# Performance work log

Measured on AMD Instinct MI355X. Metric: run time of the kernel, lower is better.

The kernel has to match this reference:

```python
import jax, jax.numpy as jnp
import numpy as np

B, C_IN, C_MID, C_OUT, L = 32, 8, 128, 128, 512
T, DT = 50, 0.5
K = T // 2 + 1  # 26
DN = ('NCH', 'OIH', 'NCH')

def conv1d_same(x, w, b):
    # zero-padded 'SAME' Conv1d, kernel size 3
    y = jax.lax.conv_general_dilated(x, w, (1,), 'SAME', dimension_numbers=DN)
    return y + b[None, :, None]

def setup_inputs() -> dict:
    key = jax.random.key(0)
    ks = jax.random.split(key, 32)
    def n(k, shape, s=0.1):
        return jax.random.normal(k, shape, dtype=jnp.float32) * s
    inp = {}
    inp['x'] = jax.random.normal(ks[0], (B, C_IN, L), dtype=jnp.float32)
    # omega encoder (3 convs + ReLU)
    inp['ow1'] = n(ks[1], (C_MID, C_IN, 3));  inp['ob1'] = jnp.zeros((C_MID,), jnp.float32)
    inp['ow2'] = n(ks[2], (C_MID, C_MID, 3)); inp['ob2'] = jnp.zeros((C_MID,), jnp.float32)
    inp['ow3'] = n(ks[3], (C_OUT, C_MID, 3)); inp['ob3'] = jnp.zeros((C_OUT,), jnp.float32)
    # alpha encoder
    inp['aw1'] = n(ks[4], (C_MID, C_IN, 3));  inp['ab1'] = jnp.zeros((C_MID,), jnp.float32)
    inp['aw2'] = n(ks[5], (C_MID, C_MID, 3)); inp['ab2'] = jnp.zeros((C_MID,), jnp.float32)
    inp['aw3'] = n(ks[6], (C_OUT, C_MID, 3)); inp['ab3'] = jnp.zeros((C_OUT,), jnp.float32)
    # hy encoder (4 convs, last Tanh)
    inp['hw1'] = n(ks[7], (C_MID, C_IN, 3));  inp['hb1'] = jnp.zeros((C_MID,), jnp.float32)
    inp['hw2'] = n(ks[8], (C_MID, C_MID, 3)); inp['hb2'] = jnp.zeros((C_MID,), jnp.float32)
    inp['hw3'] = n(ks[9], (C_MID, C_MID, 3)); inp['hb3'] = jnp.zeros((C_MID,), jnp.float32)
    inp['hw4'] = n(ks[10], (C_OUT, C_MID, 3)); inp['hb4'] = jnp.zeros((C_OUT,), jnp.float32)
    # cell circular conv weight (no bias)
    inp['wy'] = n(ks[11], (C_OUT, C_OUT, 3))
    # linear readout
    inp['fct'] = n(ks[12], (K, T))                     # fc_time: T -> K, no bias
    inp['rw1'] = n(ks[13], (64, K * C_OUT)); inp['rb1'] = jnp.zeros((64,), jnp.float32)
    inp['rw2'] = n(ks[14], (32, 64));        inp['rb2'] = jnp.zeros((32,), jnp.float32)
    inp['rw3'] = n(ks[15], (1, 32));         inp['rb3'] = jnp.zeros((1,), jnp.float32)
    return inp

def reference(x, ow1, ob1, ow2, ob2, ow3, ob3,
              aw1, ab1, aw2, ab2, aw3, ab3,
              hw1, hb1, hw2, hb2, hw3, hb3, hw4, hb4,
              wy, fct, rw1, rb1, rw2, rb2, rw3, rb3):
    relu = jax.nn.relu
    omega = relu(conv1d_same(relu(conv1d_same(relu(conv1d_same(x, ow1, ob1)), ow2, ob2)), ow3, ob3))
    alpha = relu(conv1d_same(relu(conv1d_same(relu(conv1d_same(x, aw1, ab1)), aw2, ab2)), aw3, ab3))
    h = relu(conv1d_same(x, hw1, hb1))
    h = relu(conv1d_same(h, hw2, hb2))
    h = relu(conv1d_same(h, hw3, hb3))
    hy0 = jnp.tanh(conv1d_same(h, hw4, hb4))          # (B, C_OUT, L)
    hz0 = jnp.zeros_like(hy0)

    def circ_conv(h):
        # circular padding of 1 on each side, then VALID conv (matches padding_mode='circular')
        hp = jnp.concatenate([h[..., -1:], h, h[..., :1]], axis=-1)
        return jax.lax.conv_general_dilated(hp, wy, (1,), 'VALID', dimension_numbers=DN)

    def step(carry, _):
        hy, hz = carry
        spring = jnp.tanh(circ_conv(hy))
        hz = hz + DT * (spring - omega * hy - alpha * hz)
        hy = hy + DT * hz
        return (hy, hz), hy

    (_, _), ys = jax.lax.scan(step, (hy0, hz0), None, length=T)
    y_seq = jnp.transpose(ys, (1, 0, 2, 3))           # (B, T, C_OUT, L)

    # linear readout: fc_time over T, mean over L, MLP
    fft = jnp.einsum('btcl,kt->bkcl', y_seq, fct)     # (B, K, C_OUT, L)
    feat = fft.reshape(B, K * C_OUT, L).mean(axis=2)  # (B, K*C_OUT)
    h1 = relu(feat @ rw1.T + rb1)
    h2 = relu(h1 @ rw2.T + rb2)
    logits = h2 @ rw3.T + rb3                         # (B, 1)
    return logits, y_seq
```

## Files before the change

kernel.cpp:

```cpp
#include <hip/hip_runtime.h>
#include <math.h>

#define YB (50*128*512)
#define YT (128*512)
#define DTc 0.5f

typedef __attribute__((ext_vector_type(8))) short bf16x8;
typedef __attribute__((ext_vector_type(4))) float f32x4;

__device__ __forceinline__ unsigned short f2bf(float f) {
    unsigned int u = __builtin_bit_cast(unsigned int, f);
    u += 0x7fffu + ((u >> 16) & 1u);
    return (unsigned short)(u >> 16);
}
__device__ __forceinline__ float bf2f(unsigned short h) {
    unsigned int u = ((unsigned int)h) << 16;
    return __builtin_bit_cast(float, u);
}

__device__ __forceinline__ float tanh_fast(float x) {
    float ax = fabsf(x);
    float e  = __expf(-2.f * ax);
    float r  = (1.f - e) * __builtin_amdgcn_rcpf(1.f + e);
    return __builtin_copysignf(r, x);
}

__device__ __forceinline__ void lds_sync() {
    asm volatile("s_waitcnt lgkmcnt(0)" ::: "memory");
    __builtin_amdgcn_sched_barrier(0);
    __builtin_amdgcn_s_barrier();
    __builtin_amdgcn_sched_barrier(0);
}

__device__ __forceinline__ uint4 dpp_k1(uint4 a0, uint4 a2) {
    uint4 r;
    int t;
    t = __builtin_amdgcn_update_dpp(0, (int)a0.x, 0x101, 0xF, 0xF, false);
    r.x = (unsigned)__builtin_amdgcn_update_dpp(t, (int)a2.x, 0x111, 0xF, 0xF, false);
    t = __builtin_amdgcn_update_dpp(0, (int)a0.y, 0x101, 0xF, 0xF, false);
    r.y = (unsigned)__builtin_amdgcn_update_dpp(t, (int)a2.y, 0x111, 0xF, 0xF, false);
    t = __builtin_amdgcn_update_dpp(0, (int)a0.z, 0x101, 0xF, 0xF, false);
    r.z = (unsigned)__builtin_amdgcn_update_dpp(t, (int)a2.z, 0x111, 0xF, 0xF, false);
    t = __builtin_amdgcn_update_dpp(0, (int)a0.w, 0x101, 0xF, 0xF, false);
    r.w = (unsigned)__builtin_amdgcn_update_dpp(t, (int)a2.w, 0x111, 0xF, 0xF, false);
    return r;
}

struct WSrc { const float* p[11]; };
__global__ void wprep_all_k(WSrc s, float* __restrict__ wt) {
    int idx = blockIdx.x * 256 + threadIdx.x;
    if (idx < 9216) {
        int wsel = idx / 3072, r = idx % 3072;
        int row = r >> 7, co = r & 127;
        int ci = row / 3, k = row - ci * 3;
        wt[idx] = s.p[wsel][(co * 8 + ci) * 3 + k];
    } else if (idx < 9216 + 589824) {
        int q = idx - 9216;
        int cv = q / 49152, r = q % 49152;
        int co = r / 384, kap = r % 384;
        int k = kap >> 7;
        int ci = ((kap >> 5) & 3) * 32 + (kap & 31);
        const int selmap[12] = {10, 7, 8, 9, 3, 3, 4, 4, 5, 5, 6, 6};
        float w = s.p[selmap[cv]][(co * 128 + ci) * 3 + k];
        unsigned short hv = f2bf(w);
        unsigned short ov = ((cv >= 4) && (cv & 1)) ? f2bf(w - bf2f(hv)) : hv;
        ((unsigned short*)(wt + 9216))[q] = ov;
    }
}

struct Job { const float* src; float* dst; const float* wt; const float* bias; int sbs, dbs, act; };
struct Jobs3 { Job j[3]; };

__global__ __launch_bounds__(256) void conv8x3_k(Jobs3 js) {
    int jb = blockIdx.y % 3;
    Job jo = js.j[jb];
    int b = blockIdx.z, tile = blockIdx.x, tid = threadIdx.x;
    int l0 = tile * 64;
    int tl4 = (tid & 15) * 4;
    int co0 = (tid >> 4) * 8;
    __shared__ float xs[8 * 68];
    __shared__ float wsh[24 * 128];
    const float* sb = jo.src + (size_t)b * jo.sbs;
    for (int idx = tid; idx < 8 * 66; idx += 256) {
        int ci = idx / 66, ll = idx - ci * 66;
        int gl = l0 - 1 + ll;
        xs[ci * 68 + ll] = (gl >= 0 && gl < 512) ? sb[ci * 512 + gl] : 0.f;
    }
    for (int idx = tid; idx < 24 * 128; idx += 256) wsh[idx] = jo.wt[idx];
    __syncthreads();
    float acc[8][4] = {};
    #pragma unroll
    for (int ci = 0; ci < 8; ++ci) {
        float x6[6];
        #pragma unroll
        for (int j = 0; j < 6; ++j) x6[j] = xs[ci * 68 + tl4 + j];
        #pragma unroll
        for (int k = 0; k < 3; ++k) {
            float w8[8];
            #pragma unroll
            for (int i = 0; i < 8; ++i) w8[i] = wsh[(ci * 3 + k) * 128 + co0 + i];
            #pragma unroll
            for (int i = 0; i < 8; ++i)
                #pragma unroll
                for (int j = 0; j < 4; ++j)
                    acc[i][j] = fmaf(w8[i], x6[k + j], acc[i][j]);
        }
    }
    #pragma unroll
    for (int i = 0; i < 8; ++i) {
        int co = co0 + i;
        float bv = jo.bias[co];
        float4 o;
        o.x = fmaxf(acc[i][0] + bv, 0.f);
        o.y = fmaxf(acc[i][1] + bv, 0.f);
        o.z = fmaxf(acc[i][2] + bv, 0.f);
        o.w = fmaxf(acc[i][3] + bv, 0.f);
        *(float4*)(jo.dst + (size_t)b * jo.dbs + (size_t)co * 512 + l0 + tl4) = o;
    }
}

struct UJob { const float* src; float* dst; const unsigned short* whi;
              const unsigned short* wlo; const float* bias; int sbs, dbs; };
struct UJobs3 { UJob j[3]; };

__global__ __launch_bounds__(512) void uconv_k(UJobs3 js) {
    UJob jo = js.j[blockIdx.z];
    int tile = blockIdx.x, b = blockIdx.y;
    int tid = threadIdx.x, lane = tid & 63, wid = tid >> 6;
    int lr = lane & 15, kg = lane >> 4;
    int co = wid * 16 + lr;
    int l0 = tile * 32;
    bool dual = (jo.wlo != nullptr);

    __shared__ float stage[128 * 40];
    __shared__ uint4 hiX[34 * 16];
    __shared__ uint4 loX[34 * 16];

    const bf16x8* wph = (const bf16x8*)(jo.whi + (size_t)co * 384);
    bf16x8 Bh[12];
    #pragma unroll
    for (int s = 0; s < 12; ++s) Bh[s] = wph[s * 4 + kg];

    const float* sb = jo.src + (size_t)b * jo.sbs;
    for (int i = tid; i < 1280; i += 512) {
        int c = i / 10, p4 = (i - c * 10) * 4;
        int l = l0 - 4 + p4;
        f32x4 v;
        if (l >= 0 && l <= 508) {
            v = *(const f32x4*)(sb + (size_t)c * 512 + l);
        } else {
            #pragma unroll
            for (int e = 0; e < 4; ++e) {
                int le = l + e;
                v[e] = (le >= 0 && le < 512) ? sb[(size_t)c * 512 + le] : 0.f;
            }
        }
        *(f32x4*)(stage + c * 40 + p4) = v;
    }
    __syncthreads();
    for (int i = tid; i < 34 * 16; i += 512) {
        int h = i >> 4, c8 = i & 15;
        unsigned short ph[8], pl[8];
        #pragma unroll
        for (int q = 0; q < 8; ++q) {
            float x = stage[(c8 * 8 + q) * 40 + h + 3];
            unsigned short hv = f2bf(x);
            ph[q] = hv;
            pl[q] = f2bf(x - bf2f(hv));
        }
        int sx = h * 16 + (c8 ^ (h & 7));
        hiX[sx] = *(uint4*)ph;
        if (dual) loX[sx] = *(uint4*)pl;
    }
    __syncthreads();

    f32x4 acc[2];
    acc[0] = (f32x4){0.f, 0.f, 0.f, 0.f};
    acc[1] = (f32x4){0.f, 0.f, 0.f, 0.f};
    __builtin_amdgcn_s_setprio(1);
    if (dual) {
        const bf16x8* wpl = (const bf16x8*)(jo.wlo + (size_t)co * 384);
        bf16x8 blc = wpl[kg];
        #pragma unroll
        for (int s = 0; s < 12; ++s) {
            bf16x8 Bl = blc;
            if (s < 11) blc = wpl[(s + 1) * 4 + kg];
            int k = s >> 2;
            int chunk = (s & 3) * 4 + kg;
            #pragma unroll
            for (int lt = 0; lt < 2; ++lt) {
                int arow = 16 * lt + lr + k;
                int ai = arow * 16 + ((arow & 7) ^ chunk);
                bf16x8 ah = __builtin_bit_cast(bf16x8, hiX[ai]);
                bf16x8 al = __builtin_bit_cast(bf16x8, loX[ai]);
                acc[lt] = __builtin_amdgcn_mfma_f32_16x16x32_bf16(ah, Bh[s], acc[lt], 0, 0, 0);
                acc[lt] = __builtin_amdgcn_mfma_f32_16x16x32_bf16(al, Bh[s], acc[lt], 0, 0, 0);
                acc[lt] = __builtin_amdgcn_mfma_f32_16x16x32_bf16(ah, Bl,    acc[lt], 0, 0, 0);
            }
        }
    } else {
        #pragma unroll
        for (int s = 0; s < 12; ++s) {
            int k = s >> 2;
            int chunk = (s & 3) * 4 + kg;
            #pragma unroll
            for (int lt = 0; lt < 2; ++lt) {
                int arow = 16 * lt + lr + k;
                bf16x8 ah = __builtin_bit_cast(bf16x8, hiX[arow * 16 + ((arow & 7) ^ chunk)]);
                acc[lt] = __builtin_amdgcn_mfma_f32_16x16x32_bf16(ah, Bh[s], acc[lt], 0, 0, 0);
            }
        }
    }
    __builtin_amdgcn_s_setprio(0);

    float bv = jo.bias[co];
    #pragma unroll
    for (int lt = 0; lt < 2; ++lt) {
        float v[4];
        #pragma unroll
        for (int j = 0; j < 4; ++j) v[j] = fmaxf(acc[lt][j] + bv, 0.f);
        *(f32x4*)(jo.dst + (size_t)b * jo.dbs + (size_t)co * 512 + l0 + 16 * lt + 4 * kg) = *(f32x4*)v;
    }
}

__global__ __launch_bounds__(512) void mconv_k(
    const float* __restrict__ src, int sbs,
    float* __restrict__ dst, int dbs,
    const unsigned short* __restrict__ w2,
    const float* __restrict__ bias,
    unsigned short* __restrict__ hyt)
{
    int tile = blockIdx.x, b = blockIdx.y;
    int tid = threadIdx.x, lane = tid & 63, wid = tid >> 6;
    int lr = lane & 15, kg = lane >> 4;
    int co = wid * 16 + lr;
    int l0 = tile * 32;

    __shared__ float stage[128 * 40];
    __shared__ uint4 hyX[34 * 16];

    bf16x8 Bw[12];
    {
        const bf16x8* wp = (const bf16x8*)(w2 + (size_t)co * 384);
        #pragma unroll
        for (int s = 0; s < 12; ++s) Bw[s] = wp[s * 4 + kg];
    }

    const float* sb = src + (size_t)b * sbs;
    for (int i = tid; i < 1280; i += 512) {
        int c = i / 10, p4 = (i - c * 10) * 4;
        int l = l0 - 4 + p4;
        f32x4 v;
        if (l >= 0 && l <= 508) {
            v = *(const f32x4*)(sb + (size_t)c * 512 + l);
        } else {
            #pragma unroll
            for (int e = 0; e < 4; ++e) {
                int le = l + e;
                v[e] = (le >= 0 && le < 512) ? sb[(size_t)c * 512 + le] : 0.f;
            }
        }
        *(f32x4*)(stage + c * 40 + p4) = v;
    }
    __syncthreads();
    for (int i = tid; i < 34 * 16; i += 512) {
        int h = i >> 4, c8 = i & 15;
        unsigned short pk[8];
        #pragma unroll
        for (int q = 0; q < 8; ++q) pk[q] = f2bf(stage[(c8 * 8 + q) * 40 + h + 3]);
        hyX[h * 16 + (c8 ^ (h & 7))] = *(uint4*)pk;
    }
    __syncthreads();

    f32x4 acc[2];
    acc[0] = (f32x4){0.f, 0.f, 0.f, 0.f};
    acc[1] = (f32x4){0.f, 0.f, 0.f, 0.f};
    __builtin_amdgcn_s_setprio(1);
    #pragma unroll
    for (int s = 0; s < 12; ++s) {
        int k = s >> 2;
        int chunk = (s & 3) * 4 + kg;
        bf16x8 Bf = Bw[s];
        #pragma unroll
        for (int lt = 0; lt < 2; ++lt) {
            int arow = 16 * lt + lr + k;
            bf16x8 a = __builtin_bit_cast(bf16x8, hyX[arow * 16 + ((arow & 7) ^ chunk)]);
            acc[lt] = __builtin_amdgcn_mfma_f32_16x16x32_bf16(a, Bf, acc[lt], 0, 0, 0);
        }
    }
    __builtin_amdgcn_s_setprio(0);

    float bv = bias[co];
    float vv[2][4];
    #pragma unroll
    for (int lt = 0; lt < 2; ++lt) {
        #pragma unroll
        for (int j = 0; j < 4; ++j)
            vv[lt][j] = tanh_fast(acc[lt][j] + bv);
        *(f32x4*)(dst + (size_t)b * dbs + (size_t)co * 512 + l0 + 16 * lt + 4 * kg) = *(f32x4*)vv[lt];
    }

    lds_sync();
    {
        unsigned short* t16 = (unsigned short*)hyX;
        #pragma unroll
        for (int lt = 0; lt < 2; ++lt)
            #pragma unroll
            for (int j = 0; j < 4; ++j)
                t16[(16 * lt + 4 * kg + j) * 128 + co] = f2bf(vv[lt][j]);
        lds_sync();
        int row = tid >> 4, c8 = tid & 15;
        ((uint4*)hyt)[((size_t)b * 512 + l0 + row) * 16 + c8] =
            ((uint4*)hyX)[row * 16 + c8];
    }
}

__global__ __launch_bounds__(512, 2) void chunk_k(
    const unsigned short* __restrict__ hyt_in,
    unsigned short* __restrict__ hyt_out,
    const float* __restrict__ hy_in,
    const float* __restrict__ hz_in,
    float* __restrict__ hz_out,
    const float* __restrict__ omega, const float* __restrict__ alpha,
    const unsigned short* __restrict__ w2,
    float* __restrict__ ybase,
    float* __restrict__ part, int t0, int ns)
{
    int tile = blockIdx.x, b = blockIdx.y;
    int tid = threadIdx.x, lane = tid & 63, wid = tid >> 6;
    int lr = lane & 15, kg = lane >> 4;
    int co = wid * 16 + lr;
    int l0 = tile * 32;

    __shared__ uint4 hySd[2][800];
    __shared__ float ytmp[2 * 4608];

    bf16x8 Bw[12];
    {
        const bf16x8* wp = (const bf16x8*)(w2 + (size_t)co * 384);
        #pragma unroll
        for (int s = 0; s < 12; ++s) Bw[s] = wp[s * 4 + kg];
    }

    f32x4 hyR[3], hzR[3], omR[3], alR[3];

    {
        const uint4* hsrc = (const uint4*)hyt_in + (size_t)b * 8192;
        for (int i = tid; i < 800; i += 512) {
            int h = i >> 4, c8 = i & 15;
            int l = (l0 - 9 + h) & 511;
            hySd[0][h * 16 + (c8 ^ (h & 7))] = hsrc[l * 16 + c8];
        }
    }
    {
        const float* src = hy_in + (size_t)b * YB;
        size_t ob = (size_t)b * 65536 + (size_t)co * 512;
        #pragma unroll
        for (int lt = 0; lt < 3; ++lt) {
            int l = (l0 - 8 + 16 * lt + 4 * kg) & 511;
            hyR[lt] = *(const f32x4*)(src + (size_t)co * 512 + l);
            omR[lt] = *(const f32x4*)(omega + ob + l);
            alR[lt] = *(const f32x4*)(alpha + ob + l);
            if (t0 > 0) hzR[lt] = *(const f32x4*)(hz_in + ob + l);
            else        hzR[lt] = (f32x4){0.f, 0.f, 0.f, 0.f};
        }
    }
    __syncthreads();

    for (int i = 0; i < ns; ++i) {
        const uint4* hc = &hySd[i & 1][0];
        unsigned short* hn16 = (unsigned short*)&hySd[(i + 1) & 1][0];
        float* yt = ytmp + (i & 1) * 4608;

        f32x4 acc[3];
        #pragma unroll
        for (int lt = 0; lt < 3; ++lt) acc[lt] = (f32x4){0.f, 0.f, 0.f, 0.f};
        __builtin_amdgcn_s_setprio(1);
        #pragma unroll
        for (int cs = 0; cs < 4; ++cs) {
            int chunk = cs * 4 + kg;
            bf16x8 B0 = Bw[cs], B1 = Bw[cs + 4], B2 = Bw[cs + 8];
            #pragma unroll
            for (int lt = 0; lt < 3; ++lt) {
                int r0 = 16 * lt + lr;
                int r2 = r0 + 2;
                uint4 a0 = hc[r0 * 16 + ((r0 & 7) ^ chunk)];
                uint4 a2 = hc[r2 * 16 + ((r2 & 7) ^ chunk)];
                acc[lt] = __builtin_amdgcn_mfma_f32_16x16x32_bf16(
                    __builtin_bit_cast(bf16x8, a0), B0, acc[lt], 0, 0, 0);
                acc[lt] = __builtin_amdgcn_mfma_f32_16x16x32_bf16(
                    __builtin_bit_cast(bf16x8, a2), B2, acc[lt], 0, 0, 0);
                uint4 a1 = dpp_k1(a0, a2);
                acc[lt] = __builtin_amdgcn_mfma_f32_16x16x32_bf16(
                    __builtin_bit_cast(bf16x8, a1), B1, acc[lt], 0, 0, 0);
            }
        }
        __builtin_amdgcn_s_setprio(0);

        float lsum = 0.f;
        #pragma unroll
        for (int lt = 0; lt < 3; ++lt) {
            #pragma unroll
            for (int j = 0; j < 4; ++j) {
                float spring = tanh_fast(acc[lt][j]);
                float zn = hzR[lt][j] + DTc * (spring - omR[lt][j] * hyR[lt][j] - alR[lt][j] * hzR[lt][j]);
                float hn = hyR[lt][j] + DTc * zn;
                hzR[lt][j] = zn;
                hyR[lt][j] = hn;
            }
            bool valid = (lt == 0) ? (kg >= 2) : (lt == 2) ? (kg < 2) : true;
            int r0 = 16 * lt + 4 * kg;
            if (valid) {
                *(f32x4*)(yt + co * 36 + (r0 - 8)) = hyR[lt];
                lsum += hyR[lt][0] + hyR[lt][1] + hyR[lt][2] + hyR[lt][3];
                if (i == ns - 1)
                    *(f32x4*)(hz_out + (size_t)b * 65536 + (size_t)co * 512 + l0 + (r0 - 8)) = hzR[lt];
            }
            #pragma unroll
            for (int j = 0; j < 4; ++j) {
                int rr = r0 + j + 1;
                int sidx = rr * 128 + (((co >> 3) ^ (rr & 7)) << 3) + (co & 7);
                hn16[sidx] = f2bf(hyR[lt][j]);
            }
        }
        lsum += __shfl_xor(lsum, 16);
        lsum += __shfl_xor(lsum, 32);
        if (kg == 0) part[(((size_t)b * 50 + t0 + i) * 128 + co) * 16 + tile] = lsum;

        lds_sync();

        {
            float* yrow = ybase + (size_t)b * YB + (size_t)i * YT;
            int cs2 = wid * 16 + (lane >> 3);
            int lq = (lane & 7) * 4;
            #pragma unroll
            for (int cq = 0; cq < 2; ++cq) {
                int c2 = cs2 + cq * 8;
                f32x4 v = *(const f32x4*)(yt + c2 * 36 + lq);
                *(f32x4*)(yrow + (size_t)c2 * 512 + l0 + lq) = v;
            }
        }
    }

    {
        const uint4* hl = &hySd[ns & 1][0];
        int row = tid >> 4, c8 = tid & 15;
        int h = row + 9;
        ((uint4*)hyt_out)[((size_t)b * 512 + l0 + row) * 16 + c8] =
            hl[h * 16 + (c8 ^ (h & 7))];
    }
}

__global__ __launch_bounds__(256) void readout_k(
    const float* __restrict__ part, const float* __restrict__ fct,
    const float* __restrict__ rw1, const float* __restrict__ rb1,
    const float* __restrict__ rw2, const float* __restrict__ rb2,
    const float* __restrict__ rw3, const float* __restrict__ rb3,
    float* __restrict__ out)
{
    int b = blockIdx.x, tid = threadIdx.x;
    __shared__ float ybar[50 * 128];
    __shared__ float feat[26 * 128];
    __shared__ float h1[64];
    __shared__ float h2[32];
    for (int idx = tid; idx < 50 * 128; idx += 256) {
        const float* p = part + ((size_t)b * 6400 + idx) * 16;
        float s = 0.f;
        #pragma unroll
        for (int q = 0; q < 16; ++q) s += p[q];
        ybar[idx] = s * (1.f / 512.f);
    }
    __syncthreads();
    for (int idx = tid; idx < 26 * 128; idx += 256) {
        int k = idx >> 7, c = idx & 127;
        float s = 0.f;
        for (int t = 0; t < 50; ++t) s += fct[k * 50 + t] * ybar[t * 128 + c];
        feat[idx] = s;
    }
    __syncthreads();
    {
        int j = tid >> 2, q = tid & 3;
        float s = 0.f;
        const float* r = rw1 + (size_t)j * 3328 + q * 832;
        const float* f = feat + q * 832;
        for (int i = 0; i < 832; ++i) s += f[i] * r[i];
        s += __shfl_xor(s, 1);
        s += __shfl_xor(s, 2);
        if (q == 0) h1[j] = fmaxf(s + rb1[j], 0.f);
    }
    __syncthreads();
    if (tid < 32) {
        float s = 0.f;
        for (int i = 0; i < 64; ++i) s += h1[i] * rw2[tid * 64 + i];
        h2[tid] = fmaxf(s + rb2[tid], 0.f);
    }
    __syncthreads();
    if (tid == 0) {
        float s = 0.f;
        for (int i = 0; i < 32; ++i) s += h2[i] * rw3[i];
        out[b] = s + rb3[0];
    }
}

extern "C" void kernel_launch(void* const* d_in, const int* in_sizes, int n_in,
                              void* d_out, int out_size, void* d_ws, size_t ws_size,
                              hipStream_t stream)
{
    const float* x   = (const float*)d_in[0];
    const float* ow1 = (const float*)d_in[1];  const float* ob1 = (const float*)d_in[2];
    const float* ow2 = (const float*)d_in[3];  const float* ob2 = (const float*)d_in[4];
    const float* ow3 = (const float*)d_in[5];  const float* ob3 = (const float*)d_in[6];
    const float* aw1 = (const float*)d_in[7];  const float* ab1 = (const float*)d_in[8];
    const float* aw2 = (const float*)d_in[9];  const float* ab2 = (const float*)d_in[10];
    const float* aw3 = (const float*)d_in[11]; const float* ab3 = (const float*)d_in[12];
    const float* hw1 = (const float*)d_in[13]; const float* hb1 = (const float*)d_in[14];
    const float* hw2 = (const float*)d_in[15]; const float* hb2 = (const float*)d_in[16];
    const float* hw3 = (const float*)d_in[17]; const float* hb3 = (const float*)d_in[18];
    const float* hw4 = (const float*)d_in[19]; const float* hb4 = (const float*)d_in[20];
    const float* wy  = (const float*)d_in[21];
    const float* fct = (const float*)d_in[22];
    const float* rw1 = (const float*)d_in[23]; const float* rb1 = (const float*)d_in[24];
    const float* rw2 = (const float*)d_in[25]; const float* rb2 = (const float*)d_in[26];
    const float* rw3 = (const float*)d_in[27]; const float* rb3 = (const float*)d_in[28];

    float* out  = (float*)d_out;
    float* yout = out + 32;
    float* ws   = (float*)d_ws;

    float* OMEGA = ws;
    float* ALPHA = ws + 2097152;
    float* WT    = ws + 4194304;
    float* PART  = ws + 4498432;
    float* HZ0   = ws + 7775232;
    float* HZ1   = ws + 9872384;
    unsigned short* HYT0 = (unsigned short*)(ws + 11969536);
    unsigned short* HYT1 = (unsigned short*)(ws + 13018112);

    float* To1 = yout + 44 * YT;
    float* Ta1 = yout + 45 * YT;
    float* Th1 = yout + 46 * YT;
    float* To2 = yout + 47 * YT;
    float* Ta2 = yout + 43 * YT;
    float* Th2 = yout + 49 * YT;
    float* Th3 = yout + 42 * YT;
    float* HY0 = yout + 48 * YT;

    float* OW1T = WT + 0;  float* AW1T = WT + 3072;  float* HW1T = WT + 6144;
    unsigned short* U16 = (unsigned short*)(WT + 9216);
    unsigned short* W2WY = U16;
    unsigned short* W2H2 = U16 + 49152;
    unsigned short* W2H3 = U16 + 98304;
    unsigned short* W2H4 = U16 + 147456;
    unsigned short* OW2H = U16 + 196608;  unsigned short* OW2L = U16 + 245760;
    unsigned short* OW3H = U16 + 294912;  unsigned short* OW3L = U16 + 344064;
    unsigned short* AW2H = U16 + 393216;  unsigned short* AW2L = U16 + 442368;
    unsigned short* AW3H = U16 + 491520;  unsigned short* AW3L = U16 + 540672;

    WSrc wsrc;
    wsrc.p[0] = ow1; wsrc.p[1] = aw1; wsrc.p[2] = hw1;
    wsrc.p[3] = ow2; wsrc.p[4] = ow3; wsrc.p[5] = aw2; wsrc.p[6] = aw3;
    wsrc.p[7] = hw2; wsrc.p[8] = hw3; wsrc.p[9] = hw4; wsrc.p[10] = wy;
    wprep_all_k<<<2340, 256, 0, stream>>>(wsrc, WT);

    Jobs3 d1 = {{ {x, To1, OW1T, ob1, 4096, YB, 1},
                  {x, Ta1, AW1T, ab1, 4096, YB, 1},
                  {x, Th1, HW1T, hb1, 4096, YB, 1} }};
    conv8x3_k<<<dim3(8, 3, 32), 256, 0, stream>>>(d1);

    UJobs3 u2 = {{ {To1, To2, OW2H, OW2L, ob2, YB, YB},
                   {Ta1, Ta2, AW2H, AW2L, ab2, YB, YB},
                   {Th1, Th2, W2H2, nullptr, hb2, YB, YB} }};
    uconv_k<<<dim3(16, 32, 3), 512, 0, stream>>>(u2);

    UJobs3 u3 = {{ {To2, OMEGA, OW3H, OW3L, ob3, YB, 65536},
                   {Ta2, ALPHA, AW3H, AW3L, ab3, YB, 65536},
                   {Th2, Th3, W2H3, nullptr, hb3, YB, YB} }};
    uconv_k<<<dim3(16, 32, 3), 512, 0, stream>>>(u3);

    mconv_k<<<dim3(16, 32), 512, 0, stream>>>(Th3, YB, HY0, YB, W2H4, hb4, HYT0);

    {
        int t0 = 0, c = 0;
        while (t0 < 50) {
            int ns = (50 - t0 >= 8) ? 8 : (50 - t0);
            const unsigned short* hin = (c & 1) ? HYT1 : HYT0;
            unsigned short* hout      = (c & 1) ? HYT0 : HYT1;
            const float* hyin = (t0 == 0) ? HY0 : (yout + (size_t)(t0 - 1) * YT);
            const float* hzin = (c & 1) ? HZ1 : HZ0;
            float* hzout      = (c & 1) ? HZ0 : HZ1;
            chunk_k<<<dim3(16, 32), 512, 0, stream>>>(hin, hout, hyin, hzin, hzout,
                                                      OMEGA, ALPHA, W2WY,
                                                      yout + (size_t)t0 * YT, PART, t0, ns);
            t0 += ns; ++c;
        }
    }

    readout_k<<<32, 256, 0, stream>>>(PART, fct, rw1, rb1, rw2, rb2, rw3, rb3, out);
}
```

Before: 537.2 us.

## Fuse recurrence chunks into one persistent kernel with grid barriers

Replaces the seven chunk_k launches with a single persistent kernel, recur_p_k. It runs all 50 timesteps and, every 8 steps, exchanges halo hy/hz values between tiles through global memory behind a software grid barrier. This is meant to remove the per-chunk launch overhead and the repeated reloading of weights, omega and alpha. The MFMA inner loop also drops the DPP-synthesised middle tap in favour of three direct LDS reads, which trades extra LDS traffic for fewer DPP instructions. The grid barrier assumes all 512 blocks are co-resident, so the code checks occupancy and falls back to the old chunked path if fewer than two blocks fit per CU.

After: 539.6 us. About the same (+0.4%).

```diff
diff --git a/kernel.cpp b/kernel.cpp
--- a/kernel.cpp
+++ b/kernel.cpp
@@ -4,6 +4,7 @@
 #define YB (50*128*512)
 #define YT (128*512)
 #define DTc 0.5f
+#define NBLK 512
 
 typedef __attribute__((ext_vector_type(8))) short bf16x8;
 typedef __attribute__((ext_vector_type(4))) float f32x4;
@@ -30,20 +31,6 @@
     __builtin_amdgcn_sched_barrier(0);
     __builtin_amdgcn_s_barrier();
     __builtin_amdgcn_sched_barrier(0);
-}
-
-__device__ __forceinline__ uint4 dpp_k1(uint4 a0, uint4 a2) {
-    uint4 r;
-    int t;
-    t = __builtin_amdgcn_update_dpp(0, (int)a0.x, 0x101, 0xF, 0xF, false);
-    r.x = (unsigned)__builtin_amdgcn_update_dpp(t, (int)a2.x, 0x111, 0xF, 0xF, false);
-    t = __builtin_amdgcn_update_dpp(0, (int)a0.y, 0x101, 0xF, 0xF, false);
-    r.y = (unsigned)__builtin_amdgcn_update_dpp(t, (int)a2.y, 0x111, 0xF, 0xF, false);
-    t = __builtin_amdgcn_update_dpp(0, (int)a0.z, 0x101, 0xF, 0xF, false);
-    r.z = (unsigned)__builtin_amdgcn_update_dpp(t, (int)a2.z, 0x111, 0xF, 0xF, false);
-    t = __builtin_amdgcn_update_dpp(0, (int)a0.w, 0x101, 0xF, 0xF, false);
-    r.w = (unsigned)__builtin_amdgcn_update_dpp(t, (int)a2.w, 0x111, 0xF, 0xF, false);
-    return r;
 }
 
 struct WSrc { const float* p[11]; };
@@ -315,6 +302,20 @@
     }
 }
 
+__global__ void zero_bar_k(unsigned* bar) { if (threadIdx.x < 2) bar[threadIdx.x] = 0u; }
+
+__device__ __forceinline__ void grid_barrier(unsigned* bar) {
+    unsigned g = __hip_atomic_load(bar + 1, __ATOMIC_ACQUIRE, __HIP_MEMORY_SCOPE_AGENT);
+    unsigned a = __hip_atomic_fetch_add(bar, 1u, __ATOMIC_ACQ_REL, __HIP_MEMORY_SCOPE_AGENT);
+    if (a == NBLK - 1) {
+        __hip_atomic_store(bar, 0u, __ATOMIC_RELAXED, __HIP_MEMORY_SCOPE_AGENT);
+        __hip_atomic_fetch_add(bar + 1, 1u, __ATOMIC_ACQ_REL, __HIP_MEMORY_SCOPE_AGENT);
+    } else {
+        while (__hip_atomic_load(bar + 1, __ATOMIC_ACQUIRE, __HIP_MEMORY_SCOPE_AGENT) == g)
+            __builtin_amdgcn_s_sleep(8);
+    }
+}
+
 __global__ __launch_bounds__(512, 2) void chunk_k(
     const unsigned short* __restrict__ hyt_in,
     unsigned short* __restrict__ hyt_out,
@@ -377,22 +378,15 @@
         for (int lt = 0; lt < 3; ++lt) acc[lt] = (f32x4){0.f, 0.f, 0.f, 0.f};
         __builtin_amdgcn_s_setprio(1);
         #pragma unroll
-        for (int cs = 0; cs < 4; ++cs) {
-            int chunk = cs * 4 + kg;
-            bf16x8 B0 = Bw[cs], B1 = Bw[cs + 4], B2 = Bw[cs + 8];
+        for (int s = 0; s < 12; ++s) {
+            int chunk = (s & 3) * 4 + kg;
+            int k = s >> 2;
+            bf16x8 Bf = Bw[s];
             #pragma unroll
             for (int lt = 0; lt < 3; ++lt) {
-                int r0 = 16 * lt + lr;
-                int r2 = r0 + 2;
-                uint4 a0 = hc[r0 * 16 + ((r0 & 7) ^ chunk)];
-                uint4 a2 = hc[r2 * 16 + ((r2 & 7) ^ chunk)];
-                acc[lt] = __builtin_amdgcn_mfma_f32_16x16x32_bf16(
-                    __builtin_bit_cast(bf16x8, a0), B0, acc[lt], 0, 0, 0);
-                acc[lt] = __builtin_amdgcn_mfma_f32_16x16x32_bf16(
-                    __builtin_bit_cast(bf16x8, a2), B2, acc[lt], 0, 0, 0);
-                uint4 a1 = dpp_k1(a0, a2);
-                acc[lt] = __builtin_amdgcn_mfma_f32_16x16x32_bf16(
-                    __builtin_bit_cast(bf16x8, a1), B1, acc[lt], 0, 0, 0);
+                int arow = 16 * lt + lr + k;
+                bf16x8 a = __builtin_bit_cast(bf16x8, hc[arow * 16 + ((arow & 7) ^ chunk)]);
+                acc[lt] = __builtin_amdgcn_mfma_f32_16x16x32_bf16(a, Bf, acc[lt], 0, 0, 0);
             }
         }
         __builtin_amdgcn_s_setprio(0);
@@ -448,6 +442,154 @@
         int h = row + 9;
         ((uint4*)hyt_out)[((size_t)b * 512 + l0 + row) * 16 + c8] =
             hl[h * 16 + (c8 ^ (h & 7))];
+    }
+}
+
+__global__ __launch_bounds__(512, 2) void recur_p_k(
+    const unsigned short* __restrict__ hyt_in,
+    const float* __restrict__ hy_in,
+    const float* __restrict__ omega, const float* __restrict__ alpha,
+    const unsigned short* __restrict__ w2,
+    float* __restrict__ yout,
+    float* __restrict__ hze,
+    float* __restrict__ part,
+    unsigned* __restrict__ bar)
+{
+    int tile = blockIdx.x, b = blockIdx.y;
+    int tid = threadIdx.x, lane = tid & 63, wid = tid >> 6;
+    int lr = lane & 15, kg = lane >> 4;
+    int co = wid * 16 + lr;
+    int l0 = tile * 32;
+
+    __shared__ uint4 hySd[2][800];
+    __shared__ float ytmp[2 * 4608];
+
+    bf16x8 Bw[12];
+    {
+        const bf16x8* wp = (const bf16x8*)(w2 + (size_t)co * 384);
+        #pragma unroll
+        for (int s = 0; s < 12; ++s) Bw[s] = wp[s * 4 + kg];
+    }
+
+    f32x4 hyR[3], hzR[3], omR[3], alR[3];
+
+    {
+        const uint4* hsrc = (const uint4*)hyt_in + (size_t)b * 8192;
+        for (int i = tid; i < 800; i += 512) {
+            int h = i >> 4, c8 = i & 15;
+            int l = (l0 - 9 + h) & 511;
+            hySd[0][h * 16 + (c8 ^ (h & 7))] = hsrc[l * 16 + c8];
+        }
+    }
+    {
+        const float* src = hy_in + (size_t)b * YB;
+        size_t ob = (size_t)b * 65536 + (size_t)co * 512;
+        #pragma unroll
+        for (int lt = 0; lt < 3; ++lt) {
+            int l = (l0 - 8 + 16 * lt + 4 * kg) & 511;
+            hyR[lt] = *(const f32x4*)(src + (size_t)co * 512 + l);
+            omR[lt] = *(const f32x4*)(omega + ob + l);
+            alR[lt] = *(const f32x4*)(alpha + ob + l);
+            hzR[lt] = (f32x4){0.f, 0.f, 0.f, 0.f};
+        }
+    }
+    __syncthreads();
+
+    for (int t = 0; t < 50; ++t) {
+        const uint4* hc = &hySd[t & 1][0];
+        unsigned short* hn16 = (unsigned short*)&hySd[(t + 1) & 1][0];
+        float* yt = ytmp + (t & 1) * 4608;
+
+        f32x4 acc[3];
+        #pragma unroll
+        for (int lt = 0; lt < 3; ++lt) acc[lt] = (f32x4){0.f, 0.f, 0.f, 0.f};
+        __builtin_amdgcn_s_setprio(1);
+        #pragma unroll
+        for (int s = 0; s < 12; ++s) {
+            int chunk = (s & 3) * 4 + kg;
+            int k = s >> 2;
+            bf16x8 Bf = Bw[s];
+            #pragma unroll
+            for (int lt = 0; lt < 3; ++lt) {
+                int arow = 16 * lt + lr + k;
+                bf16x8 a = __builtin_bit_cast(bf16x8, hc[arow * 16 + ((arow & 7) ^ chunk)]);
+                acc[lt] = __builtin_amdgcn_mfma_f32_16x16x32_bf16(a, Bf, acc[lt], 0, 0, 0);
+            }
+        }
+        __builtin_amdgcn_s_setprio(0);
+
+        float lsum = 0.f;
+        #pragma unroll
+        for (int lt = 0; lt < 3; ++lt) {
+            #pragma unroll
+            for (int j = 0; j < 4; ++j) {
+                float spring = tanh_fast(acc[lt][j]);
+                float zn = hzR[lt][j] + DTc * (spring - omR[lt][j] * hyR[lt][j] - alR[lt][j] * hzR[lt][j]);
+                float hn = hyR[lt][j] + DTc * zn;
+                hzR[lt][j] = zn;
+                hyR[lt][j] = hn;
+            }
+            bool valid = (lt == 0) ? (kg >= 2) : (lt == 2) ? (kg < 2) : true;
+            int r0 = 16 * lt + 4 * kg;
+            if (valid) {
+                *(f32x4*)(yt + co * 36 + (r0 - 8)) = hyR[lt];
+                lsum += hyR[lt][0] + hyR[lt][1] + hyR[lt][2] + hyR[lt][3];
+            }
+            #pragma unroll
+            for (int j = 0; j < 4; ++j) {
+                int rr = r0 + j + 1;
+                int sidx = rr * 128 + (((co >> 3) ^ (rr & 7)) << 3) + (co & 7);
+                hn16[sidx] = f2bf(hyR[lt][j]);
+            }
+        }
+        lsum += __shfl_xor(lsum, 16);
+        lsum += __shfl_xor(lsum, 32);
+        if (kg == 0) part[(((size_t)b * 50 + t) * 128 + co) * 16 + tile] = lsum;
+
+        lds_sync();
+
+        {
+            float* yrow = yout + (size_t)b * YB + (size_t)t * YT;
+            int cs2 = wid * 16 + (lane >> 3);
+            int lq = (lane & 7) * 4;
+            #pragma unroll
+            for (int cq = 0; cq < 2; ++cq) {
+                int c2 = cs2 + cq * 8;
+                f32x4 v = *(const f32x4*)(yt + c2 * 36 + lq);
+                *(f32x4*)(yrow + (size_t)c2 * 512 + l0 + lq) = v;
+            }
+        }
+
+        if ((t & 7) == 7 && t < 49) {
+            int par = (t >> 3) & 1;
+            float* hb = hze + ((((size_t)par * 32 + b) * 16 + tile) * 128 + co) * 16;
+            if (kg >= 2) *(f32x4*)(hb + (kg - 2) * 4) = hzR[0];
+            else         *(f32x4*)(hb + 8 + kg * 4)  = hzR[2];
+            __threadfence();
+            __syncthreads();
+            if (tid == 0) grid_barrier(bar);
+            __syncthreads();
+            __threadfence();
+            const float* ycur = yout + (size_t)b * YB + (size_t)t * YT;
+            if (kg < 2) {
+                hyR[0] = *(const f32x4*)(ycur + (size_t)co * 512 + ((l0 - 8 + kg * 4) & 511));
+                const float* hbl = hze + ((((size_t)par * 32 + b) * 16 + ((tile + 15) & 15)) * 128 + co) * 16;
+                hzR[0] = *(const f32x4*)(hbl + 8 + kg * 4);
+            } else {
+                hyR[2] = *(const f32x4*)(ycur + (size_t)co * 512 + ((l0 + 24 + kg * 4) & 511));
+                const float* hbr = hze + ((((size_t)par * 32 + b) * 16 + ((tile + 1) & 15)) * 128 + co) * 16;
+                hzR[2] = *(const f32x4*)(hbr + (kg - 2) * 4);
+            }
+            for (int i2 = tid; i2 < 18 * 128; i2 += 512) {
+                int hr = i2 >> 7, c = i2 & 127;
+                int h = (hr < 9) ? hr : (32 + hr);
+                int l = (l0 - 9 + h) & 511;
+                float v = ycur[(size_t)c * 512 + l];
+                int sidx = h * 128 + (((c >> 3) ^ (h & 7)) << 3) + (c & 7);
+                hn16[sidx] = f2bf(v);
+            }
+            __syncthreads();
+        }
     }
 }
 
@@ -535,6 +677,8 @@
     float* HZ1   = ws + 9872384;
     unsigned short* HYT0 = (unsigned short*)(ws + 11969536);
     unsigned short* HYT1 = (unsigned short*)(ws + 13018112);
+    unsigned* BAR = (unsigned*)(ws + 14066688);
+    float* HZE = HZ0;
 
     float* To1 = yout + 44 * YT;
     float* Ta1 = yout + 45 * YT;
@@ -579,7 +723,13 @@
 
     mconv_k<<<dim3(16, 32), 512, 0, stream>>>(Th3, YB, HY0, YB, W2H4, hb4, HYT0);
 
-    {
+    int nb = 0;
+    hipOccupancyMaxActiveBlocksPerMultiprocessor(&nb, recur_p_k, 512, 0);
+    if (nb >= 2) {
+        zero_bar_k<<<1, 64, 0, stream>>>(BAR);
+        recur_p_k<<<dim3(16, 32), 512, 0, stream>>>(HYT0, HY0, OMEGA, ALPHA, W2WY,
+                                                    yout, HZE, PART, BAR);
+    } else {
         int t0 = 0, c = 0;
         while (t0 < 50) {
             int ns = (50 - t0 >= 8) ? 8 : (50 - t0);
```
